# Kernel tuning notes

Hardware: AMD Instinct MI355X
Metric: run time of the kernel (lower is better)

Reference implementation:

```python
import jax, jax.numpy as jnp
import numpy as np

N_NODES = 50000
N_EDGES = 600000
D_IN = 128
D_HID = 16
N_CLASSES = 8


def setup_inputs() -> dict:
    key = jax.random.key(0)
    ks = jax.random.split(key, 8)
    x = jax.random.normal(ks[0], (N_NODES, D_IN), dtype=jnp.float32)
    edge_index = jax.random.randint(ks[1], (2, N_EDGES), 0, N_NODES, dtype=jnp.int64)
    s1 = 1.0 / np.sqrt(D_IN)
    s2 = 1.0 / np.sqrt(D_HID)
    W1l = jax.random.normal(ks[2], (D_IN, D_HID), dtype=jnp.float32) * s1
    b1 = jnp.zeros((D_HID,), dtype=jnp.float32)
    W1r = jax.random.normal(ks[3], (D_IN, D_HID), dtype=jnp.float32) * s1
    W2l = jax.random.normal(ks[4], (D_HID, N_CLASSES), dtype=jnp.float32) * s2
    b2 = jnp.zeros((N_CLASSES,), dtype=jnp.float32)
    W2r = jax.random.normal(ks[5], (D_HID, N_CLASSES), dtype=jnp.float32) * s2
    return {"x": x, "edge_index": edge_index, "W1l": W1l, "b1": b1, "W1r": W1r,
            "W2l": W2l, "b2": b2, "W2r": W2r}


def _sage_conv(x, src, dst, Wl, bl, Wr, num_nodes):
    # PyG SAGEConv (mean aggr, root_weight=True):
    #   out_i = lin_l(mean_{j in N(i)} x_j) + lin_r(x_i)
    msgs = x[src]                                              # [E, d] irregular gather
    agg = jax.ops.segment_sum(msgs, dst, num_segments=num_nodes)  # [N, d]
    cnt = jax.ops.segment_sum(jnp.ones((src.shape[0],), x.dtype), dst,
                              num_segments=num_nodes)          # [N]
    agg = agg / jnp.maximum(cnt, 1.0)[:, None]                 # mean (0 for isolated nodes)
    return agg @ Wl + bl + x @ Wr


def reference(x, edge_index, W1l, b1, W1r, W2l, b2, W2r):
    src, dst = edge_index[0], edge_index[1]
    n = x.shape[0]
    h = _sage_conv(x, src, dst, W1l, b1, W1r, n)
    h = jax.nn.relu(h)
    # dropout(p=0.2) is identity in eval mode
    return _sage_conv(h, src, dst, W2l, b2, W2r, n)
```

## Files before the change

### kernel.cpp

```cpp
#include <hip/hip_runtime.h>

#define NN 50000
#define NE 600000
#define DI 128
#define DH 16
#define DC 8
#define CAP 48
#define NBKT 256
#define NPB 196
#define EPB 512
#define NPART 1172
#define SCAP 16
#define NBG 782

typedef unsigned short u16;
typedef unsigned int u32;

__global__ __launch_bounds__(256) void k_part(
    const int* __restrict__ src, const int* __restrict__ dst,
    u32* __restrict__ buck, int* __restrict__ pcnt)
{
    __shared__ u32 sb[NBKT * SCAP];
    __shared__ int scnt[NBKT];
    const int tid = threadIdx.x;
    scnt[tid] = 0;
    __syncthreads();

    const int base = blockIdx.x * EPB;
#pragma unroll
    for (int k = 0; k < 2; ++k) {
        int e = base + k * 256 + tid;
        if (e < NE) {
            int s = src[e], d = dst[e];
            int b = d / NPB;
            int p = atomicAdd(&scnt[b], 1);
            if (p < SCAP) sb[b * SCAP + p] = (u32)s | ((u32)d << 16);
        }
    }
    __syncthreads();

    const size_t chunk = (size_t)blockIdx.x * NBKT * SCAP;
    for (int i = tid; i < NBKT * SCAP; i += 256) {
        int b = i >> 4, sl = i & (SCAP - 1);
        if (sl < min(scnt[b], SCAP)) buck[chunk + i] = sb[i];
    }
    pcnt[blockIdx.x * NBKT + tid] = min(scnt[tid], SCAP);
}

__global__ __launch_bounds__(256) void k_fillgemm(
    const float* __restrict__ x,
    const float* __restrict__ W1l,
    const float* __restrict__ W1r,
    const u32* __restrict__ buck, const int* __restrict__ pcnt,
    float* __restrict__ xl, float* __restrict__ xr,
    int* __restrict__ cnt, u16* __restrict__ ell)
{
    const int tid = threadIdx.x;

    if (blockIdx.x < NBKT) {
        __shared__ u16 sell[NPB * CAP];
        __shared__ int scnt2[NPB];
        const int b = blockIdx.x;
        const int nbase = b * NPB;
        for (int i = tid; i < NPB; i += 256) scnt2[i] = 0;
        __syncthreads();

        for (int seg = tid; seg < NPART; seg += 256) {
            int c = pcnt[(size_t)seg * NBKT + b];
            const u32* p = buck + ((size_t)seg * NBKT + b) * SCAP;
            for (int k = 0; k < c; ++k) {
                u32 v = p[k];
                int ld = (int)(v >> 16) - nbase;
                int q = atomicAdd(&scnt2[ld], 1);
                if (q < CAP) sell[ld * CAP + q] = (u16)(v & 0xFFFFu);
            }
        }
        __syncthreads();

        for (int i = tid; i < NPB * 6; i += 256) {
            int node = i / 6, part = i - node * 6;
            int gn = nbase + node;
            if (gn < NN)
                ((uint4*)(ell + (size_t)gn * CAP))[part] = ((const uint4*)(sell + node * CAP))[part];
        }
        for (int i = tid; i < NPB; i += 256)
            if (nbase + i < NN) cnt[nbase + i] = min(scnt2[i], CAP);
        return;
    }

    __shared__ float Wc[DI][32];
    for (int i = tid; i < DI * DH; i += 256) {
        int k = i >> 4, j = i & 15;
        Wc[k][j]      = W1l[i];
        Wc[k][j + 16] = W1r[i];
    }
    __syncthreads();

    int t = (blockIdx.x - NBKT) * 256 + tid;
    if (t >= NN * 4) return;
    int n = t >> 2, c = t & 3;
    const int co = c * 8;

    float acc[8];
#pragma unroll
    for (int j = 0; j < 8; ++j) acc[j] = 0.f;

    const float4* xrow = (const float4*)(x + (size_t)n * DI);
#pragma unroll 4
    for (int k4 = 0; k4 < DI / 4; ++k4) {
        float4 xv = xrow[k4];
#pragma unroll
        for (int kk = 0; kk < 4; ++kk) {
            const float* wr = &Wc[k4 * 4 + kk][co];
            float4 w0 = *(const float4*)(wr);
            float4 w1 = *(const float4*)(wr + 4);
            float xs = (&xv.x)[kk];
            acc[0] += xs * w0.x; acc[1] += xs * w0.y;
            acc[2] += xs * w0.z; acc[3] += xs * w0.w;
            acc[4] += xs * w1.x; acc[5] += xs * w1.y;
            acc[6] += xs * w1.z; acc[7] += xs * w1.w;
        }
    }
    float* o = (c < 2) ? (xl + (size_t)n * DH + c * 8)
                       : (xr + (size_t)n * DH + (c - 2) * 8);
    *(float4*)(o)     = make_float4(acc[0], acc[1], acc[2], acc[3]);
    *(float4*)(o + 4) = make_float4(acc[4], acc[5], acc[6], acc[7]);
}

__global__ __launch_bounds__(256) void k_l1(
    const int* __restrict__ cnt, const u16* __restrict__ ell,
    const float* __restrict__ xl, const float* __restrict__ xr,
    const float* __restrict__ b1,
    const float* __restrict__ W2l, const float* __restrict__ W2r,
    float* __restrict__ zl, float* __restrict__ zr)
{
    int t = blockIdx.x * 256 + threadIdx.x;
    if (t >= NN * 8) return;
    int n = t >> 3, sub = t & 7, s = sub >> 2, q = sub & 3;
    const int q4 = q * 4;

    int len = min(cnt[n], CAP);
    const u16* lst = ell + (size_t)n * CAP;

    float4 a0 = make_float4(0.f, 0.f, 0.f, 0.f);
    for (int j = 0; j < len; j += 8) {
        uint4 w = *(const uint4*)(lst + j);
        int i0 = (int)(s ? (w.x >> 16) : (w.x & 0xFFFFu));
        int i1 = (int)(s ? (w.y >> 16) : (w.y & 0xFFFFu));
        int i2 = (int)(s ? (w.z >> 16) : (w.z & 0xFFFFu));
        int i3 = (int)(s ? (w.w >> 16) : (w.w & 0xFFFFu));
        float m0 = (j + 0 + s < len) ? 1.f : 0.f;
        float m1 = (j + 2 + s < len) ? 1.f : 0.f;
        float m2 = (j + 4 + s < len) ? 1.f : 0.f;
        float m3 = (j + 6 + s < len) ? 1.f : 0.f;
        i0 = (j + 0 + s < len) ? i0 : 0;
        i1 = (j + 2 + s < len) ? i1 : 0;
        i2 = (j + 4 + s < len) ? i2 : 0;
        i3 = (j + 6 + s < len) ? i3 : 0;
        float4 v0 = *(const float4*)(xl + (size_t)i0 * DH + q4);
        float4 v1 = *(const float4*)(xl + (size_t)i1 * DH + q4);
        float4 v2 = *(const float4*)(xl + (size_t)i2 * DH + q4);
        float4 v3 = *(const float4*)(xl + (size_t)i3 * DH + q4);
        a0.x += v0.x*m0 + v1.x*m1 + v2.x*m2 + v3.x*m3;
        a0.y += v0.y*m0 + v1.y*m1 + v2.y*m2 + v3.y*m3;
        a0.z += v0.z*m0 + v1.z*m1 + v2.z*m2 + v3.z*m3;
        a0.w += v0.w*m0 + v1.w*m1 + v2.w*m2 + v3.w*m3;
    }
    a0.x += __shfl_xor(a0.x, 4, 64);
    a0.y += __shfl_xor(a0.y, 4, 64);
    a0.z += __shfl_xor(a0.z, 4, 64);
    a0.w += __shfl_xor(a0.w, 4, 64);

    float inv = 1.0f / fmaxf((float)len, 1.0f);
    float4 r  = *(const float4*)(xr + (size_t)n * DH + q4);
    float4 bb = *(const float4*)(b1 + q4);
    float4 hq;
    hq.x = fmaxf(a0.x * inv + bb.x + r.x, 0.f);
    hq.y = fmaxf(a0.y * inv + bb.y + r.y, 0.f);
    hq.z = fmaxf(a0.z * inv + bb.z + r.z, 0.f);
    hq.w = fmaxf(a0.w * inv + bb.w + r.w, 0.f);

    float4 p1, p2, p3;
    p1.x = __shfl_xor(hq.x, 1, 64); p1.y = __shfl_xor(hq.y, 1, 64);
    p1.z = __shfl_xor(hq.z, 1, 64); p1.w = __shfl_xor(hq.w, 1, 64);
    p2.x = __shfl_xor(hq.x, 2, 64); p2.y = __shfl_xor(hq.y, 2, 64);
    p2.z = __shfl_xor(hq.z, 2, 64); p2.w = __shfl_xor(hq.w, 2, 64);
    p3.x = __shfl_xor(p1.x, 2, 64); p3.y = __shfl_xor(p1.y, 2, 64);
    p3.z = __shfl_xor(p1.z, 2, 64); p3.w = __shfl_xor(p1.w, 2, 64);
    float4 Q[4];
#pragma unroll
    for (int jq = 0; jq < 4; ++jq) {
        int d = jq ^ q;
        Q[jq] = (d == 0) ? hq : (d == 1) ? p1 : (d == 2) ? p2 : p3;
    }

    const float* Wbase = (q < 2) ? (W2l + q * 4) : (W2r + (q - 2) * 4);
    float4 acc = make_float4(0.f, 0.f, 0.f, 0.f);
#pragma unroll
    for (int k = 0; k < DH; ++k) {
        float hk = (k < 4) ? ((const float*)&Q[0])[k & 3]
                 : (k < 8) ? ((const float*)&Q[1])[k & 3]
                 : (k < 12) ? ((const float*)&Q[2])[k & 3]
                 : ((const float*)&Q[3])[k & 3];
        float4 wv = *(const float4*)(Wbase + k * 8);
        acc.x += hk * wv.x; acc.y += hk * wv.y;
        acc.z += hk * wv.z; acc.w += hk * wv.w;
    }
    if (s == 0) {
        float* dstp = (q < 2) ? (zl + (size_t)n * DC + q * 4)
                              : (zr + (size_t)n * DC + (q - 2) * 4);
        *(float4*)dstp = acc;
    }
}

__global__ __launch_bounds__(256) void k_l2(
    const int* __restrict__ cnt, const u16* __restrict__ ell,
    const float* __restrict__ zl, const float* __restrict__ zr,
    const float* __restrict__ b2, float* __restrict__ out)
{
    int t = blockIdx.x * 256 + threadIdx.x;
    if (t >= NN * 4) return;
    int n = t >> 2, sub = t & 3, s = sub >> 1, q = sub & 1;
    const int q4 = q * 4;
    int len = min(cnt[n], CAP);
    const u16* lst = ell + (size_t)n * CAP;

    float4 a0 = make_float4(0.f, 0.f, 0.f, 0.f);
    for (int j = 0; j < len; j += 8) {
        uint4 w = *(const uint4*)(lst + j);
        int i0 = (int)(s ? (w.x >> 16) : (w.x & 0xFFFFu));
        int i1 = (int)(s ? (w.y >> 16) : (w.y & 0xFFFFu));
        int i2 = (int)(s ? (w.z >> 16) : (w.z & 0xFFFFu));
        int i3 = (int)(s ? (w.w >> 16) : (w.w & 0xFFFFu));
        float m0 = (j + 0 + s < len) ? 1.f : 0.f;
        float m1 = (j + 2 + s < len) ? 1.f : 0.f;
        float m2 = (j + 4 + s < len) ? 1.f : 0.f;
        float m3 = (j + 6 + s < len) ? 1.f : 0.f;
        i0 = (j + 0 + s < len) ? i0 : 0;
        i1 = (j + 2 + s < len) ? i1 : 0;
        i2 = (j + 4 + s < len) ? i2 : 0;
        i3 = (j + 6 + s < len) ? i3 : 0;
        float4 v0 = *(const float4*)(zl + (size_t)i0 * DC + q4);
        float4 v1 = *(const float4*)(zl + (size_t)i1 * DC + q4);
        float4 v2 = *(const float4*)(zl + (size_t)i2 * DC + q4);
        float4 v3 = *(const float4*)(zl + (size_t)i3 * DC + q4);
        a0.x += v0.x*m0 + v1.x*m1 + v2.x*m2 + v3.x*m3;
        a0.y += v0.y*m0 + v1.y*m1 + v2.y*m2 + v3.y*m3;
        a0.z += v0.z*m0 + v1.z*m1 + v2.z*m2 + v3.z*m3;
        a0.w += v0.w*m0 + v1.w*m1 + v2.w*m2 + v3.w*m3;
    }
    a0.x += __shfl_xor(a0.x, 2, 64);
    a0.y += __shfl_xor(a0.y, 2, 64);
    a0.z += __shfl_xor(a0.z, 2, 64);
    a0.w += __shfl_xor(a0.w, 2, 64);

    if (s == 0) {
        float inv = 1.0f / fmaxf((float)len, 1.0f);
        float4 r  = *(const float4*)(zr + (size_t)n * DC + q4);
        float4 bb = *(const float4*)(b2 + q4);
        float4 o;
        o.x = a0.x * inv + bb.x + r.x;
        o.y = a0.y * inv + bb.y + r.y;
        o.z = a0.z * inv + bb.z + r.z;
        o.w = a0.w * inv + bb.w + r.w;
        *(float4*)(out + (size_t)n * DC + q4) = o;
    }
}

extern "C" void kernel_launch(void* const* d_in, const int* in_sizes, int n_in,
                              void* d_out, int out_size, void* d_ws, size_t ws_size,
                              hipStream_t stream)
{
    const float* x   = (const float*)d_in[0];
    const int*   ei  = (const int*)d_in[1];
    const float* W1l = (const float*)d_in[2];
    const float* b1  = (const float*)d_in[3];
    const float* W1r = (const float*)d_in[4];
    const float* W2l = (const float*)d_in[5];
    const float* b2  = (const float*)d_in[6];
    const float* W2r = (const float*)d_in[7];
    float* out = (float*)d_out;

    const int* src = ei;
    const int* dst = ei + NE;

    float* xl  = (float*)d_ws;
    float* xr  = xl + (size_t)NN * DH;
    float* zl  = xr + (size_t)NN * DH;
    float* zr  = zl + (size_t)NN * DC;
    u16* ell   = (u16*)(zr + (size_t)NN * DC);
    int* cnt   = (int*)(ell + (size_t)NN * CAP);
    int* pcnt  = cnt + NN;
    u32* buck  = (u32*)(pcnt + (size_t)NPART * NBKT);

    k_part    <<<NPART, 256, 0, stream>>>(src, dst, buck, pcnt);
    k_fillgemm<<<NBKT + NBG, 256, 0, stream>>>(x, W1l, W1r, buck, pcnt, xl, xr, cnt, ell);
    k_l1      <<<(NN * 8 + 255) / 256, 256, 0, stream>>>(cnt, ell, xl, xr, b1, W2l, W2r, zl, zr);
    k_l2      <<<(NN * 4 + 255) / 256, 256, 0, stream>>>(cnt, ell, zl, zr, b2, out);
}
```

Baseline: 52.46 us.

## Split ELL build into four partition groups per bucket with sub-lists

The ELL-building phase used to run one block per destination bucket, and each block walked all partition segments. It is now split across four blocks per bucket, each taking every fourth segment and writing its own 16-slot sub-list and count per node. This raises parallelism in the fill stage, which had only 256 blocks doing serial segment scans. In exchange the ELL row grows to 64 slots in four groups, the aggregation kernels loop over four sub-lists with more partial-chunk masking, and capacity is now limited per group.

After: 56.20 us. 7.1% more time.

```diff
diff --git a/kernel.cpp b/kernel.cpp
--- a/kernel.cpp
+++ b/kernel.cpp
@@ -5,12 +5,15 @@
 #define DI 128
 #define DH 16
 #define DC 8
-#define CAP 48
 #define NBKT 256
 #define NPB 196
 #define EPB 512
 #define NPART 1172
 #define SCAP 16
+#define GRP 4
+#define NSEG 293
+#define RCAP 16
+#define NBB (NBKT * GRP)
 #define NBG 782
 
 typedef unsigned short u16;
@@ -47,44 +50,47 @@
     pcnt[blockIdx.x * NBKT + tid] = min(scnt[tid], SCAP);
 }
 
-__global__ __launch_bounds__(256) void k_fillgemm(
+__global__ __launch_bounds__(256) void k_buildgemm(
     const float* __restrict__ x,
     const float* __restrict__ W1l,
     const float* __restrict__ W1r,
     const u32* __restrict__ buck, const int* __restrict__ pcnt,
     float* __restrict__ xl, float* __restrict__ xr,
-    int* __restrict__ cnt, u16* __restrict__ ell)
+    int* __restrict__ cnt4, u16* __restrict__ ell)
 {
     const int tid = threadIdx.x;
 
-    if (blockIdx.x < NBKT) {
-        __shared__ u16 sell[NPB * CAP];
+    if (blockIdx.x < NBB) {
+        __shared__ u16 sell[NPB * RCAP];
         __shared__ int scnt2[NPB];
-        const int b = blockIdx.x;
+        const int b = blockIdx.x & (NBKT - 1);
+        const int g = blockIdx.x >> 8;
         const int nbase = b * NPB;
         for (int i = tid; i < NPB; i += 256) scnt2[i] = 0;
         __syncthreads();
 
-        for (int seg = tid; seg < NPART; seg += 256) {
+        for (int i = tid; i < NSEG; i += 256) {
+            int seg = g + i * GRP;
             int c = pcnt[(size_t)seg * NBKT + b];
             const u32* p = buck + ((size_t)seg * NBKT + b) * SCAP;
             for (int k = 0; k < c; ++k) {
                 u32 v = p[k];
                 int ld = (int)(v >> 16) - nbase;
                 int q = atomicAdd(&scnt2[ld], 1);
-                if (q < CAP) sell[ld * CAP + q] = (u16)(v & 0xFFFFu);
+                if (q < RCAP) sell[ld * RCAP + q] = (u16)(v & 0xFFFFu);
             }
         }
         __syncthreads();
 
-        for (int i = tid; i < NPB * 6; i += 256) {
-            int node = i / 6, part = i - node * 6;
+        for (int i = tid; i < NPB * 2; i += 256) {
+            int node = i >> 1, part = i & 1;
             int gn = nbase + node;
             if (gn < NN)
-                ((uint4*)(ell + (size_t)gn * CAP))[part] = ((const uint4*)(sell + node * CAP))[part];
+                ((uint4*)(ell + (size_t)gn * 64 + g * RCAP))[part] =
+                    ((const uint4*)(sell + node * RCAP))[part];
         }
         for (int i = tid; i < NPB; i += 256)
-            if (nbase + i < NN) cnt[nbase + i] = min(scnt2[i], CAP);
+            if (nbase + i < NN) cnt4[(size_t)(nbase + i) * GRP + g] = min(scnt2[i], RCAP);
         return;
     }
 
@@ -96,7 +102,7 @@
     }
     __syncthreads();
 
-    int t = (blockIdx.x - NBKT) * 256 + tid;
+    int t = (blockIdx.x - NBB) * 256 + tid;
     if (t >= NN * 4) return;
     int n = t >> 2, c = t & 3;
     const int co = c * 8;
@@ -128,7 +134,7 @@
 }
 
 __global__ __launch_bounds__(256) void k_l1(
-    const int* __restrict__ cnt, const u16* __restrict__ ell,
+    const int* __restrict__ cnt4, const u16* __restrict__ ell,
     const float* __restrict__ xl, const float* __restrict__ xr,
     const float* __restrict__ b1,
     const float* __restrict__ W2l, const float* __restrict__ W2r,
@@ -139,32 +145,39 @@
     int n = t >> 3, sub = t & 7, s = sub >> 2, q = sub & 3;
     const int q4 = q * 4;
 
-    int len = min(cnt[n], CAP);
-    const u16* lst = ell + (size_t)n * CAP;
+    int4 c4 = *(const int4*)(cnt4 + (size_t)n * GRP);
+    int lens[GRP] = { min(c4.x, RCAP), min(c4.y, RCAP), min(c4.z, RCAP), min(c4.w, RCAP) };
+    int len = lens[0] + lens[1] + lens[2] + lens[3];
+    const u16* lst = ell + (size_t)n * 64;
 
     float4 a0 = make_float4(0.f, 0.f, 0.f, 0.f);
-    for (int j = 0; j < len; j += 8) {
-        uint4 w = *(const uint4*)(lst + j);
-        int i0 = (int)(s ? (w.x >> 16) : (w.x & 0xFFFFu));
-        int i1 = (int)(s ? (w.y >> 16) : (w.y & 0xFFFFu));
-        int i2 = (int)(s ? (w.z >> 16) : (w.z & 0xFFFFu));
-        int i3 = (int)(s ? (w.w >> 16) : (w.w & 0xFFFFu));
-        float m0 = (j + 0 + s < len) ? 1.f : 0.f;
-        float m1 = (j + 2 + s < len) ? 1.f : 0.f;
-        float m2 = (j + 4 + s < len) ? 1.f : 0.f;
-        float m3 = (j + 6 + s < len) ? 1.f : 0.f;
-        i0 = (j + 0 + s < len) ? i0 : 0;
-        i1 = (j + 2 + s < len) ? i1 : 0;
-        i2 = (j + 4 + s < len) ? i2 : 0;
-        i3 = (j + 6 + s < len) ? i3 : 0;
-        float4 v0 = *(const float4*)(xl + (size_t)i0 * DH + q4);
-        float4 v1 = *(const float4*)(xl + (size_t)i1 * DH + q4);
-        float4 v2 = *(const float4*)(xl + (size_t)i2 * DH + q4);
-        float4 v3 = *(const float4*)(xl + (size_t)i3 * DH + q4);
-        a0.x += v0.x*m0 + v1.x*m1 + v2.x*m2 + v3.x*m3;
-        a0.y += v0.y*m0 + v1.y*m1 + v2.y*m2 + v3.y*m3;
-        a0.z += v0.z*m0 + v1.z*m1 + v2.z*m2 + v3.z*m3;
-        a0.w += v0.w*m0 + v1.w*m1 + v2.w*m2 + v3.w*m3;
+#pragma unroll
+    for (int h = 0; h < GRP; ++h) {
+        int lenh = lens[h];
+        const u16* L = lst + h * RCAP;
+        for (int j = 0; j < lenh; j += 8) {
+            uint4 w = *(const uint4*)(L + j);
+            int i0 = (int)(s ? (w.x >> 16) : (w.x & 0xFFFFu));
+            int i1 = (int)(s ? (w.y >> 16) : (w.y & 0xFFFFu));
+            int i2 = (int)(s ? (w.z >> 16) : (w.z & 0xFFFFu));
+            int i3 = (int)(s ? (w.w >> 16) : (w.w & 0xFFFFu));
+            float m0 = (j + 0 + s < lenh) ? 1.f : 0.f;
+            float m1 = (j + 2 + s < lenh) ? 1.f : 0.f;
+            float m2 = (j + 4 + s < lenh) ? 1.f : 0.f;
+            float m3 = (j + 6 + s < lenh) ? 1.f : 0.f;
+            i0 = (j + 0 + s < lenh) ? i0 : 0;
+            i1 = (j + 2 + s < lenh) ? i1 : 0;
+            i2 = (j + 4 + s < lenh) ? i2 : 0;
+            i3 = (j + 6 + s < lenh) ? i3 : 0;
+            float4 v0 = *(const float4*)(xl + (size_t)i0 * DH + q4);
+            float4 v1 = *(const float4*)(xl + (size_t)i1 * DH + q4);
+            float4 v2 = *(const float4*)(xl + (size_t)i2 * DH + q4);
+            float4 v3 = *(const float4*)(xl + (size_t)i3 * DH + q4);
+            a0.x += v0.x*m0 + v1.x*m1 + v2.x*m2 + v3.x*m3;
+            a0.y += v0.y*m0 + v1.y*m1 + v2.y*m2 + v3.y*m3;
+            a0.z += v0.z*m0 + v1.z*m1 + v2.z*m2 + v3.z*m3;
+            a0.w += v0.w*m0 + v1.w*m1 + v2.w*m2 + v3.w*m3;
+        }
     }
     a0.x += __shfl_xor(a0.x, 4, 64);
     a0.y += __shfl_xor(a0.y, 4, 64);
@@ -214,7 +227,7 @@
 }
 
 __global__ __launch_bounds__(256) void k_l2(
-    const int* __restrict__ cnt, const u16* __restrict__ ell,
+    const int* __restrict__ cnt4, const u16* __restrict__ ell,
     const float* __restrict__ zl, const float* __restrict__ zr,
     const float* __restrict__ b2, float* __restrict__ out)
 {
@@ -222,32 +235,39 @@
     if (t >= NN * 4) return;
     int n = t >> 2, sub = t & 3, s = sub >> 1, q = sub & 1;
     const int q4 = q * 4;
-    int len = min(cnt[n], CAP);
-    const u16* lst = ell + (size_t)n * CAP;
+    int4 c4 = *(const int4*)(cnt4 + (size_t)n * GRP);
+    int lens[GRP] = { min(c4.x, RCAP), min(c4.y, RCAP), min(c4.z, RCAP), min(c4.w, RCAP) };
+    int len = lens[0] + lens[1] + lens[2] + lens[3];
+    const u16* lst = ell + (size_t)n * 64;
 
     float4 a0 = make_float4(0.f, 0.f, 0.f, 0.f);
-    for (int j = 0; j < len; j += 8) {
-        uint4 w = *(const uint4*)(lst + j);
-        int i0 = (int)(s ? (w.x >> 16) : (w.x & 0xFFFFu));
-        int i1 = (int)(s ? (w.y >> 16) : (w.y & 0xFFFFu));
-        int i2 = (int)(s ? (w.z >> 16) : (w.z & 0xFFFFu));
-        int i3 = (int)(s ? (w.w >> 16) : (w.w & 0xFFFFu));
-        float m0 = (j + 0 + s < len) ? 1.f : 0.f;
-        float m1 = (j + 2 + s < len) ? 1.f : 0.f;
-        float m2 = (j + 4 + s < len) ? 1.f : 0.f;
-        float m3 = (j + 6 + s < len) ? 1.f : 0.f;
-        i0 = (j + 0 + s < len) ? i0 : 0;
-        i1 = (j + 2 + s < len) ? i1 : 0;
-        i2 = (j + 4 + s < len) ? i2 : 0;
-        i3 = (j + 6 + s < len) ? i3 : 0;
-        float4 v0 = *(const float4*)(zl + (size_t)i0 * DC + q4);
-        float4 v1 = *(const float4*)(zl + (size_t)i1 * DC + q4);
-        float4 v2 = *(const float4*)(zl + (size_t)i2 * DC + q4);
-        float4 v3 = *(const float4*)(zl + (size_t)i3 * DC + q4);
-        a0.x += v0.x*m0 + v1.x*m1 + v2.x*m2 + v3.x*m3;
-        a0.y += v0.y*m0 + v1.y*m1 + v2.y*m2 + v3.y*m3;
-        a0.z += v0.z*m0 + v1.z*m1 + v2.z*m2 + v3.z*m3;
-        a0.w += v0.w*m0 + v1.w*m1 + v2.w*m2 + v3.w*m3;
+#pragma unroll
+    for (int h = 0; h < GRP; ++h) {
+        int lenh = lens[h];
+        const u16* L = lst + h * RCAP;
+        for (int j = 0; j < lenh; j += 8) {
+            uint4 w = *(const uint4*)(L + j);
+            int i0 = (int)(s ? (w.x >> 16) : (w.x & 0xFFFFu));
+            int i1 = (int)(s ? (w.y >> 16) : (w.y & 0xFFFFu));
+            int i2 = (int)(s ? (w.z >> 16) : (w.z & 0xFFFFu));
+            int i3 = (int)(s ? (w.w >> 16) : (w.w & 0xFFFFu));
+            float m0 = (j + 0 + s < lenh) ? 1.f : 0.f;
+            float m1 = (j + 2 + s < lenh) ? 1.f : 0.f;
+            float m2 = (j + 4 + s < lenh) ? 1.f : 0.f;
+            float m3 = (j + 6 + s < lenh) ? 1.f : 0.f;
+            i0 = (j + 0 + s < lenh) ? i0 : 0;
+            i1 = (j + 2 + s < lenh) ? i1 : 0;
+            i2 = (j + 4 + s < lenh) ? i2 : 0;
+            i3 = (j + 6 + s < lenh) ? i3 : 0;
+            float4 v0 = *(const float4*)(zl + (size_t)i0 * DC + q4);
+            float4 v1 = *(const float4*)(zl + (size_t)i1 * DC + q4);
+            float4 v2 = *(const float4*)(zl + (size_t)i2 * DC + q4);
+            float4 v3 = *(const float4*)(zl + (size_t)i3 * DC + q4);
+            a0.x += v0.x*m0 + v1.x*m1 + v2.x*m2 + v3.x*m3;
+            a0.y += v0.y*m0 + v1.y*m1 + v2.y*m2 + v3.y*m3;
+            a0.z += v0.z*m0 + v1.z*m1 + v2.z*m2 + v3.z*m3;
+            a0.w += v0.w*m0 + v1.w*m1 + v2.w*m2 + v3.w*m3;
+        }
     }
     a0.x += __shfl_xor(a0.x, 2, 64);
     a0.y += __shfl_xor(a0.y, 2, 64);
@@ -289,12 +309,12 @@
     float* zl  = xr + (size_t)NN * DH;
     float* zr  = zl + (size_t)NN * DC;
     u16* ell   = (u16*)(zr + (size_t)NN * DC);
-    int* cnt   = (int*)(ell + (size_t)NN * CAP);
-    int* pcnt  = cnt + NN;
+    int* cnt4  = (int*)(ell + (size_t)NN * 64);
+    int* pcnt  = cnt4 + (size_t)NN * GRP;
     u32* buck  = (u32*)(pcnt + (size_t)NPART * NBKT);
 
-    k_part    <<<NPART, 256, 0, stream>>>(src, dst, buck, pcnt);
-    k_fillgemm<<<NBKT + NBG, 256, 0, stream>>>(x, W1l, W1r, buck, pcnt, xl, xr, cnt, ell);
-    k_l1      <<<(NN * 8 + 255) / 256, 256, 0, stream>>>(cnt, ell, xl, xr, b1, W2l, W2r, zl, zr);
-    k_l2      <<<(NN * 4 + 255) / 256, 256, 0, stream>>>(cnt, ell, zl, zr, b2, out);
-}
+    k_part     <<<NPART, 256, 0, stream>>>(src, dst, buck, pcnt);
+    k_buildgemm<<<NBB + NBG, 256, 0, stream>>>(x, W1l, W1r, buck, pcnt, xl, xr, cnt4, ell);
+    k_l1       <<<(NN * 8 + 255) / 256, 256, 0, stream>>>(cnt4, ell, xl, xr, b1, W2l, W2r, zl, zr);
+    k_l2       <<<(NN * 4 + 255) / 256, 256, 0, stream>>>(cnt4, ell, zl, zr, b2, out);
+}
```

## Fuse edge partitioning with GEMM and ELL build with layer-1 aggregation

Applied to the files above, without the earlier changes.

Merges the edge-partition kernel with the layer-1 dense GEMM into one launch. It also fuses the per-bucket ELL construction with the layer-1 mean aggregation, ReLU and layer-2 projection, using 1024-thread blocks that read neighbor lists from shared memory. This removes a kernel launch and a global round trip for the ELL lists in layer 1. In exchange, the layer-1 gather now runs on only 256 large blocks, which may reduce latency hiding compared with the many small blocks used before.

Result: faster. 47.04 us (-10.3%).

```diff
diff --git a/kernel.cpp b/kernel.cpp
--- a/kernel.cpp
+++ b/kernel.cpp
@@ -16,79 +16,46 @@
 typedef unsigned short u16;
 typedef unsigned int u32;
 
-__global__ __launch_bounds__(256) void k_part(
-    const int* __restrict__ src, const int* __restrict__ dst,
-    u32* __restrict__ buck, int* __restrict__ pcnt)
-{
-    __shared__ u32 sb[NBKT * SCAP];
-    __shared__ int scnt[NBKT];
-    const int tid = threadIdx.x;
-    scnt[tid] = 0;
-    __syncthreads();
-
-    const int base = blockIdx.x * EPB;
-#pragma unroll
-    for (int k = 0; k < 2; ++k) {
-        int e = base + k * 256 + tid;
-        if (e < NE) {
-            int s = src[e], d = dst[e];
-            int b = d / NPB;
-            int p = atomicAdd(&scnt[b], 1);
-            if (p < SCAP) sb[b * SCAP + p] = (u32)s | ((u32)d << 16);
-        }
-    }
-    __syncthreads();
-
-    const size_t chunk = (size_t)blockIdx.x * NBKT * SCAP;
-    for (int i = tid; i < NBKT * SCAP; i += 256) {
-        int b = i >> 4, sl = i & (SCAP - 1);
-        if (sl < min(scnt[b], SCAP)) buck[chunk + i] = sb[i];
-    }
-    pcnt[blockIdx.x * NBKT + tid] = min(scnt[tid], SCAP);
-}
-
-__global__ __launch_bounds__(256) void k_fillgemm(
+__global__ __launch_bounds__(256) void k_partgemm(
     const float* __restrict__ x,
     const float* __restrict__ W1l,
     const float* __restrict__ W1r,
-    const u32* __restrict__ buck, const int* __restrict__ pcnt,
-    float* __restrict__ xl, float* __restrict__ xr,
-    int* __restrict__ cnt, u16* __restrict__ ell)
+    const int* __restrict__ src, const int* __restrict__ dst,
+    u32* __restrict__ buck, int* __restrict__ pcnt,
+    float* __restrict__ xl, float* __restrict__ xr)
 {
+    __shared__ __align__(16) char smem[NBKT * SCAP * 4 + NBKT * 4];
     const int tid = threadIdx.x;
 
-    if (blockIdx.x < NBKT) {
-        __shared__ u16 sell[NPB * CAP];
-        __shared__ int scnt2[NPB];
-        const int b = blockIdx.x;
-        const int nbase = b * NPB;
-        for (int i = tid; i < NPB; i += 256) scnt2[i] = 0;
+    if (blockIdx.x < NPART) {
+        u32* sb  = (u32*)smem;
+        int* scnt = (int*)(smem + NBKT * SCAP * 4);
+        scnt[tid] = 0;
         __syncthreads();
 
-        for (int seg = tid; seg < NPART; seg += 256) {
-            int c = pcnt[(size_t)seg * NBKT + b];
-            const u32* p = buck + ((size_t)seg * NBKT + b) * SCAP;
-            for (int k = 0; k < c; ++k) {
-                u32 v = p[k];
-                int ld = (int)(v >> 16) - nbase;
-                int q = atomicAdd(&scnt2[ld], 1);
-                if (q < CAP) sell[ld * CAP + q] = (u16)(v & 0xFFFFu);
+        const int base = blockIdx.x * EPB;
+#pragma unroll
+        for (int k = 0; k < 2; ++k) {
+            int e = base + k * 256 + tid;
+            if (e < NE) {
+                int s = src[e], d = dst[e];
+                int b = d / NPB;
+                int p = atomicAdd(&scnt[b], 1);
+                if (p < SCAP) sb[b * SCAP + p] = (u32)s | ((u32)d << 16);
             }
         }
         __syncthreads();
 
-        for (int i = tid; i < NPB * 6; i += 256) {
-            int node = i / 6, part = i - node * 6;
-            int gn = nbase + node;
-            if (gn < NN)
-                ((uint4*)(ell + (size_t)gn * CAP))[part] = ((const uint4*)(sell + node * CAP))[part];
-        }
-        for (int i = tid; i < NPB; i += 256)
-            if (nbase + i < NN) cnt[nbase + i] = min(scnt2[i], CAP);
+        const size_t chunk = (size_t)blockIdx.x * NBKT * SCAP;
+        for (int i = tid; i < NBKT * SCAP; i += 256) {
+            int b = i >> 4, sl = i & (SCAP - 1);
+            if (sl < min(scnt[b], SCAP)) buck[chunk + i] = sb[i];
+        }
+        pcnt[blockIdx.x * NBKT + tid] = min(scnt[tid], SCAP);
         return;
     }
 
-    __shared__ float Wc[DI][32];
+    float (*Wc)[32] = (float(*)[32])smem;
     for (int i = tid; i < DI * DH; i += 256) {
         int k = i >> 4, j = i & 15;
         Wc[k][j]      = W1l[i];
@@ -96,7 +63,7 @@
     }
     __syncthreads();
 
-    int t = (blockIdx.x - NBKT) * 256 + tid;
+    int t = (blockIdx.x - NPART) * 256 + tid;
     if (t >= NN * 4) return;
     int n = t >> 2, c = t & 3;
     const int co = c * 8;
@@ -127,89 +94,125 @@
     *(float4*)(o + 4) = make_float4(acc[4], acc[5], acc[6], acc[7]);
 }
 
-__global__ __launch_bounds__(256) void k_l1(
-    const int* __restrict__ cnt, const u16* __restrict__ ell,
+__global__ __launch_bounds__(1024) void k_buildl1(
+    const u32* __restrict__ buck, const int* __restrict__ pcnt,
     const float* __restrict__ xl, const float* __restrict__ xr,
     const float* __restrict__ b1,
     const float* __restrict__ W2l, const float* __restrict__ W2r,
+    int* __restrict__ cnt, u16* __restrict__ ell,
     float* __restrict__ zl, float* __restrict__ zr)
 {
-    int t = blockIdx.x * 256 + threadIdx.x;
-    if (t >= NN * 8) return;
-    int n = t >> 3, sub = t & 7, s = sub >> 2, q = sub & 3;
-    const int q4 = q * 4;
-
-    int len = min(cnt[n], CAP);
-    const u16* lst = ell + (size_t)n * CAP;
-
-    float4 a0 = make_float4(0.f, 0.f, 0.f, 0.f);
-    for (int j = 0; j < len; j += 8) {
-        uint4 w = *(const uint4*)(lst + j);
-        int i0 = (int)(s ? (w.x >> 16) : (w.x & 0xFFFFu));
-        int i1 = (int)(s ? (w.y >> 16) : (w.y & 0xFFFFu));
-        int i2 = (int)(s ? (w.z >> 16) : (w.z & 0xFFFFu));
-        int i3 = (int)(s ? (w.w >> 16) : (w.w & 0xFFFFu));
-        float m0 = (j + 0 + s < len) ? 1.f : 0.f;
-        float m1 = (j + 2 + s < len) ? 1.f : 0.f;
-        float m2 = (j + 4 + s < len) ? 1.f : 0.f;
-        float m3 = (j + 6 + s < len) ? 1.f : 0.f;
-        i0 = (j + 0 + s < len) ? i0 : 0;
-        i1 = (j + 2 + s < len) ? i1 : 0;
-        i2 = (j + 4 + s < len) ? i2 : 0;
-        i3 = (j + 6 + s < len) ? i3 : 0;
-        float4 v0 = *(const float4*)(xl + (size_t)i0 * DH + q4);
-        float4 v1 = *(const float4*)(xl + (size_t)i1 * DH + q4);
-        float4 v2 = *(const float4*)(xl + (size_t)i2 * DH + q4);
-        float4 v3 = *(const float4*)(xl + (size_t)i3 * DH + q4);
-        a0.x += v0.x*m0 + v1.x*m1 + v2.x*m2 + v3.x*m3;
-        a0.y += v0.y*m0 + v1.y*m1 + v2.y*m2 + v3.y*m3;
-        a0.z += v0.z*m0 + v1.z*m1 + v2.z*m2 + v3.z*m3;
-        a0.w += v0.w*m0 + v1.w*m1 + v2.w*m2 + v3.w*m3;
-    }
-    a0.x += __shfl_xor(a0.x, 4, 64);
-    a0.y += __shfl_xor(a0.y, 4, 64);
-    a0.z += __shfl_xor(a0.z, 4, 64);
-    a0.w += __shfl_xor(a0.w, 4, 64);
-
-    float inv = 1.0f / fmaxf((float)len, 1.0f);
-    float4 r  = *(const float4*)(xr + (size_t)n * DH + q4);
-    float4 bb = *(const float4*)(b1 + q4);
-    float4 hq;
-    hq.x = fmaxf(a0.x * inv + bb.x + r.x, 0.f);
-    hq.y = fmaxf(a0.y * inv + bb.y + r.y, 0.f);
-    hq.z = fmaxf(a0.z * inv + bb.z + r.z, 0.f);
-    hq.w = fmaxf(a0.w * inv + bb.w + r.w, 0.f);
-
-    float4 p1, p2, p3;
-    p1.x = __shfl_xor(hq.x, 1, 64); p1.y = __shfl_xor(hq.y, 1, 64);
-    p1.z = __shfl_xor(hq.z, 1, 64); p1.w = __shfl_xor(hq.w, 1, 64);
-    p2.x = __shfl_xor(hq.x, 2, 64); p2.y = __shfl_xor(hq.y, 2, 64);
-    p2.z = __shfl_xor(hq.z, 2, 64); p2.w = __shfl_xor(hq.w, 2, 64);
-    p3.x = __shfl_xor(p1.x, 2, 64); p3.y = __shfl_xor(p1.y, 2, 64);
-    p3.z = __shfl_xor(p1.z, 2, 64); p3.w = __shfl_xor(p1.w, 2, 64);
-    float4 Q[4];
-#pragma unroll
-    for (int jq = 0; jq < 4; ++jq) {
-        int d = jq ^ q;
-        Q[jq] = (d == 0) ? hq : (d == 1) ? p1 : (d == 2) ? p2 : p3;
-    }
-
-    const float* Wbase = (q < 2) ? (W2l + q * 4) : (W2r + (q - 2) * 4);
-    float4 acc = make_float4(0.f, 0.f, 0.f, 0.f);
-#pragma unroll
-    for (int k = 0; k < DH; ++k) {
-        float hk = (k < 4) ? ((const float*)&Q[0])[k & 3]
-                 : (k < 8) ? ((const float*)&Q[1])[k & 3]
-                 : (k < 12) ? ((const float*)&Q[2])[k & 3]
-                 : ((const float*)&Q[3])[k & 3];
-        float4 wv = *(const float4*)(Wbase + k * 8);
-        acc.x += hk * wv.x; acc.y += hk * wv.y;
-        acc.z += hk * wv.z; acc.w += hk * wv.w;
-    }
-    if (s == 0) {
-        float* dstp = (q < 2) ? (zl + (size_t)n * DC + q * 4)
-                              : (zr + (size_t)n * DC + (q - 2) * 4);
-        *(float4*)dstp = acc;
+    __shared__ u16 sell[NPB * CAP];
+    __shared__ int scnt2[NPB];
+    const int tid = threadIdx.x;
+    const int b = blockIdx.x;
+    const int nbase = b * NPB;
+
+    for (int i = tid; i < NPB; i += 1024) scnt2[i] = 0;
+    __syncthreads();
+
+    for (int seg = tid; seg < NPART; seg += 1024) {
+        int c = pcnt[(size_t)seg * NBKT + b];
+        const u32* p = buck + ((size_t)seg * NBKT + b) * SCAP;
+        for (int k = 0; k < c; ++k) {
+            u32 v = p[k];
+            int ld = (int)(v >> 16) - nbase;
+            int q = atomicAdd(&scnt2[ld], 1);
+            if (q < CAP) sell[ld * CAP + q] = (u16)(v & 0xFFFFu);
+        }
+    }
+    __syncthreads();
+
+    for (int i = tid; i < NPB * 6; i += 1024) {
+        int node = i / 6, part = i - node * 6;
+        int gn = nbase + node;
+        if (gn < NN)
+            ((uint4*)(ell + (size_t)gn * CAP))[part] = ((const uint4*)(sell + node * CAP))[part];
+    }
+    for (int i = tid; i < NPB; i += 1024)
+        if (nbase + i < NN) cnt[nbase + i] = min(scnt2[i], CAP);
+
+#pragma unroll
+    for (int k = 0; k < 2; ++k) {
+        int unit = k * 1024 + tid;
+        if (unit >= NPB * 8) break;
+        int nl = unit >> 3, sub = tid & 7, s = sub >> 2, q = sub & 3;
+        int n = nbase + nl;
+        if (n >= NN) continue;
+        const int q4 = q * 4;
+
+        int len = min(scnt2[nl], CAP);
+        const u16* lst = sell + nl * CAP;
+
+        float4 a0 = make_float4(0.f, 0.f, 0.f, 0.f);
+        for (int j = 0; j < len; j += 8) {
+            uint4 w = *(const uint4*)(lst + j);
+            int i0 = (int)(s ? (w.x >> 16) : (w.x & 0xFFFFu));
+            int i1 = (int)(s ? (w.y >> 16) : (w.y & 0xFFFFu));
+            int i2 = (int)(s ? (w.z >> 16) : (w.z & 0xFFFFu));
+            int i3 = (int)(s ? (w.w >> 16) : (w.w & 0xFFFFu));
+            float m0 = (j + 0 + s < len) ? 1.f : 0.f;
+            float m1 = (j + 2 + s < len) ? 1.f : 0.f;
+            float m2 = (j + 4 + s < len) ? 1.f : 0.f;
+            float m3 = (j + 6 + s < len) ? 1.f : 0.f;
+            i0 = (j + 0 + s < len) ? i0 : 0;
+            i1 = (j + 2 + s < len) ? i1 : 0;
+            i2 = (j + 4 + s < len) ? i2 : 0;
+            i3 = (j + 6 + s < len) ? i3 : 0;
+            float4 v0 = *(const float4*)(xl + (size_t)i0 * DH + q4);
+            float4 v1 = *(const float4*)(xl + (size_t)i1 * DH + q4);
+            float4 v2 = *(const float4*)(xl + (size_t)i2 * DH + q4);
+            float4 v3 = *(const float4*)(xl + (size_t)i3 * DH + q4);
+            a0.x += v0.x*m0 + v1.x*m1 + v2.x*m2 + v3.x*m3;
+            a0.y += v0.y*m0 + v1.y*m1 + v2.y*m2 + v3.y*m3;
+            a0.z += v0.z*m0 + v1.z*m1 + v2.z*m2 + v3.z*m3;
+            a0.w += v0.w*m0 + v1.w*m1 + v2.w*m2 + v3.w*m3;
+        }
+        a0.x += __shfl_xor(a0.x, 4, 64);
+        a0.y += __shfl_xor(a0.y, 4, 64);
+        a0.z += __shfl_xor(a0.z, 4, 64);
+        a0.w += __shfl_xor(a0.w, 4, 64);
+
+        float inv = 1.0f / fmaxf((float)len, 1.0f);
+        float4 r  = *(const float4*)(xr + (size_t)n * DH + q4);
+        float4 bb = *(const float4*)(b1 + q4);
+        float4 hq;
+        hq.x = fmaxf(a0.x * inv + bb.x + r.x, 0.f);
+        hq.y = fmaxf(a0.y * inv + bb.y + r.y, 0.f);
+        hq.z = fmaxf(a0.z * inv + bb.z + r.z, 0.f);
+        hq.w = fmaxf(a0.w * inv + bb.w + r.w, 0.f);
+
+        float4 p1, p2, p3;
+        p1.x = __shfl_xor(hq.x, 1, 64); p1.y = __shfl_xor(hq.y, 1, 64);
+        p1.z = __shfl_xor(hq.z, 1, 64); p1.w = __shfl_xor(hq.w, 1, 64);
+        p2.x = __shfl_xor(hq.x, 2, 64); p2.y = __shfl_xor(hq.y, 2, 64);
+        p2.z = __shfl_xor(hq.z, 2, 64); p2.w = __shfl_xor(hq.w, 2, 64);
+        p3.x = __shfl_xor(p1.x, 2, 64); p3.y = __shfl_xor(p1.y, 2, 64);
+        p3.z = __shfl_xor(p1.z, 2, 64); p3.w = __shfl_xor(p1.w, 2, 64);
+        float4 Q[4];
+#pragma unroll
+        for (int jq = 0; jq < 4; ++jq) {
+            int d = jq ^ q;
+            Q[jq] = (d == 0) ? hq : (d == 1) ? p1 : (d == 2) ? p2 : p3;
+        }
+
+        const float* Wbase = (q < 2) ? (W2l + q * 4) : (W2r + (q - 2) * 4);
+        float4 acc = make_float4(0.f, 0.f, 0.f, 0.f);
+#pragma unroll
+        for (int kk = 0; kk < DH; ++kk) {
+            float hk = (kk < 4) ? ((const float*)&Q[0])[kk & 3]
+                     : (kk < 8) ? ((const float*)&Q[1])[kk & 3]
+                     : (kk < 12) ? ((const float*)&Q[2])[kk & 3]
+                     : ((const float*)&Q[3])[kk & 3];
+            float4 wv = *(const float4*)(Wbase + kk * 8);
+            acc.x += hk * wv.x; acc.y += hk * wv.y;
+            acc.z += hk * wv.z; acc.w += hk * wv.w;
+        }
+        if (s == 0) {
+            float* dstp = (q < 2) ? (zl + (size_t)n * DC + q * 4)
+                                  : (zr + (size_t)n * DC + (q - 2) * 4);
+            *(float4*)dstp = acc;
+        }
     }
 }
 
@@ -293,8 +296,7 @@
     int* pcnt  = cnt + NN;
     u32* buck  = (u32*)(pcnt + (size_t)NPART * NBKT);
 
-    k_part    <<<NPART, 256, 0, stream>>>(src, dst, buck, pcnt);
-    k_fillgemm<<<NBKT + NBG, 256, 0, stream>>>(x, W1l, W1r, buck, pcnt, xl, xr, cnt, ell);
-    k_l1      <<<(NN * 8 + 255) / 256, 256, 0, stream>>>(cnt, ell, xl, xr, b1, W2l, W2r, zl, zr);
+    k_partgemm<<<NPART + NBG, 256, 0, stream>>>(x, W1l, W1r, src, dst, buck, pcnt, xl, xr);
+    k_buildl1 <<<NBKT, 1024, 0, stream>>>(buck, pcnt, xl, xr, b1, W2l, W2r, cnt, ell, zl, zr);
     k_l2      <<<(NN * 4 + 255) / 256, 256, 0, stream>>>(cnt, ell, zl, zr, b2, out);
 }
```
